# Kernel tuning notes

Measured on AMD Instinct MI355X. Metric: run time of the kernel, lower is better.

The kernel has to match this reference:

```python
import jax, jax.numpy as jnp
import numpy as np

B, N, C = 64, 1024, 128


def setup_inputs() -> dict:
    key = jax.random.key(0)
    k1, k2, k3, k4, k5, k6 = jax.random.split(key, 6)
    adj_vals = jax.random.uniform(k1, (B, N, N), dtype=jnp.float32)
    mask = jax.random.uniform(k2, (B, N, N)) < 0.1
    adjacent = jnp.where(mask, adj_vals, 0.0)
    annotations = jax.random.normal(k3, (B, N, C), dtype=jnp.float32)
    # GraphConvolution bias, shape (1,1,C)
    gc_bias = jax.random.normal(k4, (1, 1, C), dtype=jnp.float32) * 0.05
    # Keras GRU params (reset_after=True default): kernel (C,3C), recurrent (C,3C), bias (2,3C)
    kernel = jax.random.normal(k5, (C, 3 * C), dtype=jnp.float32) / np.sqrt(C)
    recurrent_kernel = jax.random.normal(k6, (C, 3 * C), dtype=jnp.float32) / np.sqrt(C)
    gru_bias = jnp.zeros((2, 3 * C), dtype=jnp.float32)
    return {"adjacent": adjacent, "annotations": annotations, "gc_bias": gc_bias,
            "kernel": kernel, "recurrent_kernel": recurrent_kernel, "gru_bias": gru_bias}


def reference(adjacent, annotations, gc_bias, kernel, recurrent_kernel, gru_bias):
    # GraphConvolution: per-graph adj @ annotations, batched, + bias
    v = jnp.einsum('bij,bjc->bic', adjacent, annotations) + gc_bias  # [B,N,C]
    b, n, c = v.shape
    x = v.reshape(-1, c)            # visible states, one GRU step each
    h = annotations.reshape(-1, c)  # initial hidden states
    # single-step Keras GRU (reset_after=True)
    mx = x @ kernel + gru_bias[0]
    mh = h @ recurrent_kernel + gru_bias[1]
    xz, xr, xh = jnp.split(mx, 3, axis=-1)
    hz, hr, hh_in = jnp.split(mh, 3, axis=-1)
    z = jax.nn.sigmoid(xz + hz)
    r = jax.nn.sigmoid(xr + hr)
    hh = jnp.tanh(xh + r * hh_in)
    out = z * h + (1.0 - z) * hh
    return out.reshape(b, n, c)
```

## Files before the change

kernel.cpp:

```cpp
#include <hip/hip_runtime.h>

typedef unsigned short ushort_t;
typedef __attribute__((ext_vector_type(8))) short bf16x8;
typedef __attribute__((ext_vector_type(8))) unsigned short u16x8;
typedef __attribute__((ext_vector_type(4))) float f32x4;

#define B_ 64
#define N_ 1024
#define C_ 128

static __device__ __forceinline__ unsigned short f2bf(float f) {
  union { float f; unsigned int i; } v; v.f = f;
  unsigned int i = v.i;
  return (unsigned short)((i + 0x7FFFu + ((i >> 16) & 1u)) >> 16);
}
static __device__ __forceinline__ void split1(float x, ushort_t& h, ushort_t& l) {
  union { float f; unsigned int i; } u; u.f = x;
  h = (ushort_t)(u.i >> 16);
  union { unsigned int i; float f; } t; t.i = u.i & 0xFFFF0000u;
  union { float f; unsigned int i; } w; w.f = x - t.f;
  l = (ushort_t)(w.i >> 16);
}
static __device__ __forceinline__ bf16x8 as_bf(u16x8 v) {
  union { u16x8 u; bf16x8 b; } x; x.u = v; return x.b;
}
static __device__ __forceinline__ void gload_lds16(const void* g, void* l) {
  __builtin_amdgcn_global_load_lds((const __attribute__((address_space(1))) void*)g,
                                   (__attribute__((address_space(3))) void*)l,
                                   16, 0, 0);
}

__global__ __launch_bounds__(256) void tsplit(const float* __restrict__ src,
                                              ushort_t* __restrict__ dh,
                                              ushort_t* __restrict__ dl,
                                              int rows, int cols, long sb, long db) {
  __shared__ float tile[64][65];
  const int t = threadIdx.x;
  src += (long)blockIdx.z * sb;
  dh  += (long)blockIdx.z * db;
  dl  += (long)blockIdx.z * db;
  const int r0 = blockIdx.y * 64, c0 = blockIdx.x * 64;
#pragma unroll
  for (int p = 0; p < 4; ++p) {
    int row = p * 16 + (t >> 4), c4 = (t & 15) * 4;
    f32x4 v = *(const f32x4*)(src + (long)(r0 + row) * cols + c0 + c4);
#pragma unroll
    for (int j = 0; j < 4; ++j) tile[row][c4 + j] = v[j];
  }
  __syncthreads();
  const int oc = t >> 2;
#pragma unroll
  for (int p = 0; p < 2; ++p) {
    int ck = (t & 3) + p * 4;
    u16x8 vh, vl;
#pragma unroll
    for (int j = 0; j < 8; ++j) {
      ushort_t hj, lj;
      split1(tile[ck * 8 + j][oc], hj, lj);
      vh[j] = hj; vl[j] = lj;
    }
    long o = (long)(c0 + oc) * rows + r0 + ck * 8;
    *(u16x8*)(dh + o) = vh;
    *(u16x8*)(dl + o) = vl;
  }
}

__global__ __launch_bounds__(256, 2) void gc_gru(const float* __restrict__ adj,
                                                 const ushort_t* __restrict__ annTh,
                                                 const ushort_t* __restrict__ annTl,
                                                 const float* __restrict__ ann,
                                                 const float* __restrict__ gcb,
                                                 const ushort_t* __restrict__ kTh,
                                                 const ushort_t* __restrict__ kTl,
                                                 const ushort_t* __restrict__ rTh,
                                                 const float* __restrict__ gb,
                                                 float* __restrict__ out) {
  __shared__ __align__(16) float vlds[128 * 132];
  ushort_t* ldsAh = (ushort_t*)vlds;
  ushort_t* ldsAl = ldsAh + 128 * 64;
  ushort_t* ldsBh = ldsAl + 128 * 64;
  ushort_t* ldsBl = ldsBh + 128 * 64;

  const int tid = threadIdx.x;
  const int w = tid >> 6, lane = tid & 63;
  const int wr = w >> 1, wc = w & 1;
  const int swz = (blockIdx.x & 7) * 64 + (blockIdx.x >> 3);
  const int b = swz >> 3;
  const int m0 = (swz & 7) * 128;

  const float*    adjb = adj   + ((long)b * N_ + m0) * N_;
  const ushort_t* aThb = annTh + (long)b * C_ * N_;
  const ushort_t* aTlb = annTl + (long)b * C_ * N_;

  const int srow8 = lane >> 3;
  const int klog  = ((lane & 7) * 16) ^ (srow8 << 4);
  const int fr = lane & 15;
  const int kg = lane >> 4;

  f32x4 acc[4][4] = {};

  for (int k0 = 0; k0 < N_; k0 += 64) {
#pragma unroll
    for (int jj = 0; jj < 4; ++jj) {
      int j = w * 4 + jj;
      long so = (long)(j * 8 + srow8) * N_ + k0 + (klog >> 1);
      gload_lds16(aThb + so, (void*)&ldsBh[j * 512]);
      gload_lds16(aTlb + so, (void*)&ldsBl[j * 512]);
    }
#pragma unroll
    for (int q = 0; q < 4; ++q) {
      int ch = q * 256 + tid;
      int row = ch >> 3, ce = ch & 7;
      const float* g = adjb + (long)row * N_ + k0 + ce * 8;
      f32x4 a0 = *(const f32x4*)g;
      f32x4 a1 = *(const f32x4*)(g + 4);
      u16x8 vh, vl;
#pragma unroll
      for (int j = 0; j < 4; ++j) {
        ushort_t hj, lj;
        split1(a0[j], hj, lj); vh[j] = hj; vl[j] = lj;
        split1(a1[j], hj, lj); vh[4 + j] = hj; vl[4 + j] = lj;
      }
      int kb = (ce * 16) ^ ((row & 7) << 4);
      *(u16x8*)((char*)ldsAh + row * 128 + kb) = vh;
      *(u16x8*)((char*)ldsAl + row * 128 + kb) = vl;
    }
    __syncthreads();
#pragma unroll
    for (int kk = 0; kk < 2; ++kk) {
      bf16x8 ah[4], al[4], bh[4], bl[4];
#pragma unroll
      for (int mi = 0; mi < 4; ++mi) {
        int row = wr * 64 + mi * 16 + fr;
        int kb = (kk * 64 + kg * 16) ^ ((row & 7) << 4);
        ah[mi] = *(const bf16x8*)((const char*)ldsAh + row * 128 + kb);
        al[mi] = *(const bf16x8*)((const char*)ldsAl + row * 128 + kb);
      }
#pragma unroll
      for (int ni = 0; ni < 4; ++ni) {
        int row = wc * 64 + ni * 16 + fr;
        int kb = (kk * 64 + kg * 16) ^ ((row & 7) << 4);
        bh[ni] = *(const bf16x8*)((const char*)ldsBh + row * 128 + kb);
        bl[ni] = *(const bf16x8*)((const char*)ldsBl + row * 128 + kb);
      }
#pragma unroll
      for (int mi = 0; mi < 4; ++mi)
#pragma unroll
        for (int ni = 0; ni < 4; ++ni) {
          acc[mi][ni] = __builtin_amdgcn_mfma_f32_16x16x32_bf16(ah[mi], bh[ni], acc[mi][ni], 0, 0, 0);
          acc[mi][ni] = __builtin_amdgcn_mfma_f32_16x16x32_bf16(al[mi], bh[ni], acc[mi][ni], 0, 0, 0);
          acc[mi][ni] = __builtin_amdgcn_mfma_f32_16x16x32_bf16(ah[mi], bl[ni], acc[mi][ni], 0, 0, 0);
        }
    }
    __syncthreads();
  }

#pragma unroll
  for (int ni = 0; ni < 4; ++ni) {
    int col = wc * 64 + ni * 16 + fr;
    float bias = gcb[col];
#pragma unroll
    for (int mi = 0; mi < 4; ++mi) {
      int row = wr * 64 + mi * 16 + kg * 4;
#pragma unroll
      for (int r = 0; r < 4; ++r)
        vlds[(row + r) * 132 + col] = acc[mi][ni][r] + bias;
    }
  }
  __syncthreads();

  const long grow = (long)b * N_ + m0 + w * 32;

  bf16x8 xh[2][4], xl[2][4], hh[2][4];
#pragma unroll
  for (int s = 0; s < 2; ++s)
#pragma unroll
    for (int kk = 0; kk < 4; ++kk) {
      int lrow = w * 32 + s * 16 + fr;
      int k0 = kk * 32 + kg * 8;
      f32x4 x0 = *(const f32x4*)&vlds[lrow * 132 + k0];
      f32x4 x1 = *(const f32x4*)&vlds[lrow * 132 + k0 + 4];
      u16x8 th, tl;
#pragma unroll
      for (int j = 0; j < 4; ++j) {
        ushort_t hj, lj;
        split1(x0[j], hj, lj); th[j] = hj; tl[j] = lj;
        split1(x1[j], hj, lj); th[4 + j] = hj; tl[4 + j] = lj;
      }
      xh[s][kk] = as_bf(th); xl[s][kk] = as_bf(tl);
      const float* hrow = ann + (grow + s * 16 + fr) * C_ + k0;
      f32x4 h0 = *(const f32x4*)hrow;
      f32x4 h1 = *(const f32x4*)(hrow + 4);
      u16x8 hv;
#pragma unroll
      for (int j = 0; j < 4; ++j) { hv[j] = f2bf(h0[j]); hv[4 + j] = f2bf(h1[j]); }
      hh[s][kk] = as_bf(hv);
    }

#define GATE(G, AK0, AK1, AR0, AR1)                                                         \
  do {                                                                                      \
    const ushort_t* kh_ = kTh + (long)((G) * C_ + cb) * C_;                                 \
    const ushort_t* kl_ = kTl + (long)((G) * C_ + cb) * C_;                                 \
    const ushort_t* rh_ = rTh + (long)((G) * C_ + cb) * C_;                                 \
    bf16x8 KH[4], KL[4], RH[4];                                                             \
    _Pragma("unroll")                                                                       \
    for (int kk = 0; kk < 4; ++kk) {                                                        \
      int o_ = kk * 32 + kg * 8;                                                            \
      KH[kk] = *(const bf16x8*)(kh_ + o_);                                                  \
      KL[kk] = *(const bf16x8*)(kl_ + o_);                                                  \
      RH[kk] = *(const bf16x8*)(rh_ + o_);                                                  \
    }                                                                                       \
    _Pragma("unroll")                                                                       \
    for (int kk = 0; kk < 4; ++kk) {                                                        \
      AK0 = __builtin_amdgcn_mfma_f32_16x16x32_bf16(xh[0][kk], KH[kk], AK0, 0, 0, 0);       \
      AK1 = __builtin_amdgcn_mfma_f32_16x16x32_bf16(xh[1][kk], KH[kk], AK1, 0, 0, 0);       \
      AK0 = __builtin_amdgcn_mfma_f32_16x16x32_bf16(xl[0][kk], KH[kk], AK0, 0, 0, 0);       \
      AK1 = __builtin_amdgcn_mfma_f32_16x16x32_bf16(xl[1][kk], KH[kk], AK1, 0, 0, 0);       \
      AK0 = __builtin_amdgcn_mfma_f32_16x16x32_bf16(xh[0][kk], KL[kk], AK0, 0, 0, 0);       \
      AK1 = __builtin_amdgcn_mfma_f32_16x16x32_bf16(xh[1][kk], KL[kk], AK1, 0, 0, 0);       \
    }                                                                                       \
    _Pragma("unroll")                                                                       \
    for (int kk = 0; kk < 4; ++kk) {                                                        \
      AR0 = __builtin_amdgcn_mfma_f32_16x16x32_bf16(hh[0][kk], RH[kk], AR0, 0, 0, 0);       \
      AR1 = __builtin_amdgcn_mfma_f32_16x16x32_bf16(hh[1][kk], RH[kk], AR1, 0, 0, 0);       \
    }                                                                                       \
  } while (0)

#pragma unroll 1
  for (int n = 0; n < 8; ++n) {
    const int cb = n * 16 + fr;
    f32x4 az0 = {}, az1 = {}, ar0 = {}, ar1 = {}, ax0 = {}, ax1 = {}, ah0 = {}, ah1 = {};
    GATE(0, az0, az1, az0, az1);
    GATE(1, ar0, ar1, ar0, ar1);
    GATE(2, ax0, ax1, ah0, ah1);

    const float bz  = gb[cb] + gb[384 + cb];
    const float brr = gb[128 + cb] + gb[384 + 128 + cb];
    const float bxh = gb[256 + cb];
    const float bhi = gb[384 + 256 + cb];
#pragma unroll
    for (int s = 0; s < 2; ++s) {
      const f32x4& az_ = s ? az1 : az0;
      const f32x4& ar_ = s ? ar1 : ar0;
      const f32x4& ax_ = s ? ax1 : ax0;
      const f32x4& ah_ = s ? ah1 : ah0;
#pragma unroll
      for (int r = 0; r < 4; ++r) {
        long row = grow + s * 16 + kg * 4 + r;
        float hval = ann[row * C_ + cb];
        float zz = 1.f / (1.f + __expf(-(az_[r] + bz)));
        float rr = 1.f / (1.f + __expf(-(ar_[r] + brr)));
        float hpre = ax_[r] + bxh + rr * (ah_[r] + bhi);
        hpre = fminf(fmaxf(hpre, -15.f), 15.f);
        float e2 = __expf(2.f * hpre);
        float th = (e2 - 1.f) / (e2 + 1.f);
        out[row * C_ + cb] = zz * hval + (1.f - zz) * th;
      }
    }
  }
#undef GATE
}

extern "C" void kernel_launch(void* const* d_in, const int* in_sizes, int n_in,
                              void* d_out, int out_size, void* d_ws, size_t ws_size,
                              hipStream_t stream) {
  const float* adj = (const float*)d_in[0];
  const float* ann = (const float*)d_in[1];
  const float* gcb = (const float*)d_in[2];
  const float* ker = (const float*)d_in[3];
  const float* rk  = (const float*)d_in[4];
  const float* gb  = (const float*)d_in[5];
  float* out = (float*)d_out;

  char* ws = (char*)d_ws;
  ushort_t* annTh = (ushort_t*)(ws);
  ushort_t* annTl = (ushort_t*)(ws + 16777216);
  ushort_t* kTh   = (ushort_t*)(ws + 33554432);
  ushort_t* kTl   = (ushort_t*)(ws + 33652736);
  ushort_t* rTh   = (ushort_t*)(ws + 33751040);
  ushort_t* rTl   = (ushort_t*)(ws + 33849344);

  hipLaunchKernelGGL(tsplit, dim3(2, 16, 64), dim3(256), 0, stream,
                     ann, annTh, annTl, 1024, 128, (long)1024 * 128, (long)128 * 1024);
  hipLaunchKernelGGL(tsplit, dim3(6, 2, 1), dim3(256), 0, stream,
                     ker, kTh, kTl, 128, 384, 0L, 0L);
  hipLaunchKernelGGL(tsplit, dim3(6, 2, 1), dim3(256), 0, stream,
                     rk, rTh, rTl, 128, 384, 0L, 0L);
  hipLaunchKernelGGL(gc_gru, dim3(512), dim3(256), 0, stream,
                     adj, annTh, annTl, ann, gcb, kTh, kTl, rTh, gb, out);
}
```

Measured before the change: 165.0 us.

## Load adjacency directly into MFMA registers and double-buffer annotation tiles

The adjacency operand is now loaded from global memory straight into registers in the MFMA fragment layout and split into bf16 hi/lo pairs in-register, so it no longer goes through LDS. The annotation B tiles are double-buffered in LDS, with the next tile's async loads and register prefetches issued during the current tile's compute, leaving one barrier per iteration instead of two. This aims to hide global latency and cut LDS traffic. In exchange, register pressure rises (16 f32x4 prefetch registers) and redundant A loads occur, because the two column-waves each load the same adjacency rows.

```diff
diff --git a/kernel.cpp b/kernel.cpp
--- a/kernel.cpp
+++ b/kernel.cpp
@@ -76,10 +76,7 @@
                                                  const float* __restrict__ gb,
                                                  float* __restrict__ out) {
   __shared__ __align__(16) float vlds[128 * 132];
-  ushort_t* ldsAh = (ushort_t*)vlds;
-  ushort_t* ldsAl = ldsAh + 128 * 64;
-  ushort_t* ldsBh = ldsAl + 128 * 64;
-  ushort_t* ldsBl = ldsBh + 128 * 64;
+  ushort_t* ldsB = (ushort_t*)vlds;
 
   const int tid = threadIdx.x;
   const int w = tid >> 6, lane = tid & 63;
@@ -88,7 +85,6 @@
   const int b = swz >> 3;
   const int m0 = (swz & 7) * 128;
 
-  const float*    adjb = adj   + ((long)b * N_ + m0) * N_;
   const ushort_t* aThb = annTh + (long)b * C_ * N_;
   const ushort_t* aTlb = annTl + (long)b * C_ * N_;
 
@@ -97,63 +93,81 @@
   const int fr = lane & 15;
   const int kg = lane >> 4;
 
+  const float* aBase = adj + ((long)b * N_ + m0 + wr * 64 + fr) * N_ + kg * 8;
+
   f32x4 acc[4][4] = {};
-
-  for (int k0 = 0; k0 < N_; k0 += 64) {
-#pragma unroll
-    for (int jj = 0; jj < 4; ++jj) {
-      int j = w * 4 + jj;
-      long so = (long)(j * 8 + srow8) * N_ + k0 + (klog >> 1);
-      gload_lds16(aThb + so, (void*)&ldsBh[j * 512]);
-      gload_lds16(aTlb + so, (void*)&ldsBl[j * 512]);
-    }
-#pragma unroll
-    for (int q = 0; q < 4; ++q) {
-      int ch = q * 256 + tid;
-      int row = ch >> 3, ce = ch & 7;
-      const float* g = adjb + (long)row * N_ + k0 + ce * 8;
-      f32x4 a0 = *(const f32x4*)g;
-      f32x4 a1 = *(const f32x4*)(g + 4);
-      u16x8 vh, vl;
-#pragma unroll
-      for (int j = 0; j < 4; ++j) {
-        ushort_t hj, lj;
-        split1(a0[j], hj, lj); vh[j] = hj; vl[j] = lj;
-        split1(a1[j], hj, lj); vh[4 + j] = hj; vl[4 + j] = lj;
-      }
-      int kb = (ce * 16) ^ ((row & 7) << 4);
-      *(u16x8*)((char*)ldsAh + row * 128 + kb) = vh;
-      *(u16x8*)((char*)ldsAl + row * 128 + kb) = vl;
-    }
+  f32x4 Aa[8], Ab[8];
+
+#define STAGE(CUR, T)                                                          \
+  _Pragma("unroll")                                                            \
+  for (int jj = 0; jj < 4; ++jj) {                                             \
+    int j_ = w * 4 + jj;                                                       \
+    long so_ = (long)(j_ * 8 + srow8) * N_ + (T) * 64 + (klog >> 1);           \
+    gload_lds16(aThb + so_, (void*)(ldsB + ((CUR) * 2 + 0) * 8192 + j_ * 512));\
+    gload_lds16(aTlb + so_, (void*)(ldsB + ((CUR) * 2 + 1) * 8192 + j_ * 512));\
+  }
+
+#define LOADA(DST, T, KK)                                                      \
+  _Pragma("unroll")                                                            \
+  for (int mi = 0; mi < 4; ++mi) {                                             \
+    const float* g_ = aBase + (long)mi * 16 * N_ + (T) * 64 + (KK) * 32;       \
+    DST[2 * mi]     = *(const f32x4*)g_;                                       \
+    DST[2 * mi + 1] = *(const f32x4*)(g_ + 4);                                 \
+  }
+
+#define COMPUTE(CUR, KK, AREG)                                                 \
+  {                                                                            \
+    bf16x8 bh_[4], bl_[4], ah_[4], al_[4];                                     \
+    _Pragma("unroll")                                                          \
+    for (int ni = 0; ni < 4; ++ni) {                                           \
+      int row_ = wc * 64 + ni * 16 + fr;                                       \
+      int kb_ = ((KK) * 64 + kg * 16) ^ ((row_ & 7) << 4);                     \
+      bh_[ni] = *(const bf16x8*)((const char*)ldsB + ((CUR) * 2 + 0) * 16384 + row_ * 128 + kb_); \
+      bl_[ni] = *(const bf16x8*)((const char*)ldsB + ((CUR) * 2 + 1) * 16384 + row_ * 128 + kb_); \
+    }                                                                          \
+    _Pragma("unroll")                                                          \
+    for (int mi = 0; mi < 4; ++mi) {                                           \
+      u16x8 vh_, vl_;                                                          \
+      _Pragma("unroll")                                                        \
+      for (int j = 0; j < 4; ++j) {                                            \
+        ushort_t hj_, lj_;                                                     \
+        split1(AREG[2 * mi][j], hj_, lj_);     vh_[j] = hj_;     vl_[j] = lj_; \
+        split1(AREG[2 * mi + 1][j], hj_, lj_); vh_[4 + j] = hj_; vl_[4 + j] = lj_; \
+      }                                                                        \
+      ah_[mi] = as_bf(vh_); al_[mi] = as_bf(vl_);                              \
+    }                                                                          \
+    _Pragma("unroll")                                                          \
+    for (int mi = 0; mi < 4; ++mi)                                             \
+      _Pragma("unroll")                                                        \
+      for (int ni = 0; ni < 4; ++ni) {                                         \
+        acc[mi][ni] = __builtin_amdgcn_mfma_f32_16x16x32_bf16(ah_[mi], bh_[ni], acc[mi][ni], 0, 0, 0); \
+        acc[mi][ni] = __builtin_amdgcn_mfma_f32_16x16x32_bf16(al_[mi], bh_[ni], acc[mi][ni], 0, 0, 0); \
+        acc[mi][ni] = __builtin_amdgcn_mfma_f32_16x16x32_bf16(ah_[mi], bl_[ni], acc[mi][ni], 0, 0, 0); \
+      }                                                                        \
+  }
+
+  STAGE(0, 0)
+  LOADA(Aa, 0, 0)
+  LOADA(Ab, 0, 1)
+  __syncthreads();
+
+#pragma unroll 1
+  for (int t = 0; t < 15; ++t) {
+    const int cur = t & 1;
+    STAGE(cur ^ 1, t + 1)
+    COMPUTE(cur, 0, Aa)
+    LOADA(Aa, t + 1, 0)
+    COMPUTE(cur, 1, Ab)
+    LOADA(Ab, t + 1, 1)
     __syncthreads();
-#pragma unroll
-    for (int kk = 0; kk < 2; ++kk) {
-      bf16x8 ah[4], al[4], bh[4], bl[4];
-#pragma unroll
-      for (int mi = 0; mi < 4; ++mi) {
-        int row = wr * 64 + mi * 16 + fr;
-        int kb = (kk * 64 + kg * 16) ^ ((row & 7) << 4);
-        ah[mi] = *(const bf16x8*)((const char*)ldsAh + row * 128 + kb);
-        al[mi] = *(const bf16x8*)((const char*)ldsAl + row * 128 + kb);
-      }
-#pragma unroll
-      for (int ni = 0; ni < 4; ++ni) {
-        int row = wc * 64 + ni * 16 + fr;
-        int kb = (kk * 64 + kg * 16) ^ ((row & 7) << 4);
-        bh[ni] = *(const bf16x8*)((const char*)ldsBh + row * 128 + kb);
-        bl[ni] = *(const bf16x8*)((const char*)ldsBl + row * 128 + kb);
-      }
-#pragma unroll
-      for (int mi = 0; mi < 4; ++mi)
-#pragma unroll
-        for (int ni = 0; ni < 4; ++ni) {
-          acc[mi][ni] = __builtin_amdgcn_mfma_f32_16x16x32_bf16(ah[mi], bh[ni], acc[mi][ni], 0, 0, 0);
-          acc[mi][ni] = __builtin_amdgcn_mfma_f32_16x16x32_bf16(al[mi], bh[ni], acc[mi][ni], 0, 0, 0);
-          acc[mi][ni] = __builtin_amdgcn_mfma_f32_16x16x32_bf16(ah[mi], bl[ni], acc[mi][ni], 0, 0, 0);
-        }
-    }
-    __syncthreads();
-  }
+  }
+  COMPUTE(1, 0, Aa)
+  COMPUTE(1, 1, Ab)
+  __syncthreads();
+
+#undef STAGE
+#undef LOADA
+#undef COMPUTE
 
 #pragma unroll
   for (int ni = 0; ni < 4; ++ni) {
```

Result: slower. 181.1 us (+9.7%).
